# Kernel tuning notes

Measured on AMD Instinct MI355X. Metric: run time of the kernel, lower is better.

The kernel has to match this reference:

```python
import jax, jax.numpy as jnp
import numpy as np

D_MODEL = 1024
N_HEAD = 16
D_K = D_MODEL // N_HEAD
B, S = 2, 2048


def setup_inputs() -> dict:
    key = jax.random.key(0)
    ks = jax.random.split(key, 12)
    sc = 1.0 / np.sqrt(D_MODEL)
    return {
        "q": jax.random.normal(ks[0], (B, S, D_MODEL), jnp.float32),
        "k": jax.random.normal(ks[1], (B, S, D_MODEL), jnp.float32),
        "v": jax.random.normal(ks[2], (B, S, D_MODEL), jnp.float32),
        "mask": jax.random.randint(ks[3], (B, S, S), 0, 2, jnp.int32),
        # learned params (torch Linear convention: y = x @ W + b with W pre-transposed)
        "wq": jax.random.normal(ks[4], (D_MODEL, D_MODEL), jnp.float32) * sc,
        "bq": jax.random.normal(ks[5], (D_MODEL,), jnp.float32) * sc,
        "wk": jax.random.normal(ks[6], (D_MODEL, D_MODEL), jnp.float32) * sc,  # no bias
        "wv": jax.random.normal(ks[7], (D_MODEL, D_MODEL), jnp.float32) * sc,
        "bv": jax.random.normal(ks[8], (D_MODEL,), jnp.float32) * sc,
        "wf": jax.random.normal(ks[9], (D_MODEL, D_MODEL), jnp.float32) * sc,
        "bf": jax.random.normal(ks[10], (D_MODEL,), jnp.float32) * sc,
    }


def reference(q, k, v, mask, wq, bq, wk, wv, bv, wf, bf):
    bs = q.shape[0]
    temperature = jnp.asarray(D_K ** 0.5, q.dtype)
    # projections -> [b, h, s, d_k]
    qh = (q @ wq + bq).reshape(bs, -1, N_HEAD, D_K).transpose(0, 2, 1, 3)
    kh = (k @ wk).reshape(bs, -1, N_HEAD, D_K).transpose(0, 2, 1, 3)
    vh = (v @ wv + bv).reshape(bs, -1, N_HEAD, D_K).transpose(0, 2, 1, 3)
    # scores [b, h, sq, sk]
    attn = jnp.einsum("bhqd,bhkd->bhqk", qh, kh) / temperature
    m0 = (mask[:, None, :, :] == 0)  # mask==0 -> masked out, broadcast over heads
    attn = jnp.where(m0, -jnp.inf, attn)
    attn = jax.nn.softmax(attn, axis=-1)
    attn = jnp.where(m0, 0.0, attn)
    out = jnp.einsum("bhqk,bhkd->bhqd", attn, vh)
    out = out.transpose(0, 2, 1, 3).reshape(bs, -1, D_MODEL)
    return out @ wf + bf  # dropout is identity in eval mode
```

## Files before the change

### kernel.cpp

```cpp
#include <hip/hip_runtime.h>

#define D_MODEL 1024
#define NHEAD   16
#define DK      64
#define BATCH   2
#define SEQ     2048

typedef __attribute__((ext_vector_type(8))) short bf16x8;
typedef __attribute__((ext_vector_type(4))) short bf16x4;
typedef __attribute__((ext_vector_type(4))) float f32x4;
typedef __attribute__((ext_vector_type(2))) int i32x2;

#define QSCALE 0.18033688011f

__device__ __forceinline__ unsigned short f2b(float x) {
  unsigned u = __builtin_bit_cast(unsigned, x);
  u = (u + 0x7fffu + ((u >> 16) & 1u)) >> 16;
  return (unsigned short)u;
}
__device__ __forceinline__ unsigned short f2b_rhu(float x) {
  return (unsigned short)((__builtin_bit_cast(unsigned, x) + 0x8000u) >> 16);
}
__device__ __forceinline__ int pk2(float a, float b) {
  unsigned ua = __builtin_bit_cast(unsigned, a) + 0x8000u;
  unsigned ub = __builtin_bit_cast(unsigned, b) + 0x8000u;
  return (int)__builtin_amdgcn_perm(ub, ua, 0x07060302u);
}
__device__ __forceinline__ int pk2u(unsigned ua, unsigned ub) {
  return (int)__builtin_amdgcn_perm(ub + 0x8000u, ua + 0x8000u, 0x07060302u);
}

typedef const __attribute__((address_space(1))) void* gas_p;
typedef __attribute__((address_space(3))) void* las_p;
__device__ __forceinline__ void gll16(const void* g, void* l) {
  __builtin_amdgcn_global_load_lds((gas_p)g, (las_p)l, 16, 0, 0);
}

__device__ __forceinline__ f32x4 mfma16(bf16x4 a, bf16x4 b, f32x4 c) {
#if __has_builtin(__builtin_amdgcn_mfma_f32_16x16x16bf16_1k)
  return __builtin_amdgcn_mfma_f32_16x16x16bf16_1k(a, b, c, 0, 0, 0);
#else
  f32x4 d;
  asm("v_mfma_f32_16x16x16_bf16 %0, %1, %2, %3" : "=v"(d) : "v"(a), "v"(b), "v"(c));
  return d;
#endif
}

__global__ __launch_bounds__(256) void prep_kernel(
    const float* __restrict__ q, const float* __restrict__ k, const float* __restrict__ v,
    unsigned short* __restrict__ qb, unsigned short* __restrict__ kb,
    unsigned short* __restrict__ vb,
    const float* __restrict__ wq, const float* __restrict__ wk,
    const float* __restrict__ wv, const float* __restrict__ wf,
    unsigned short* __restrict__ wqt, unsigned short* __restrict__ wkt,
    unsigned short* __restrict__ wvt, unsigned short* __restrict__ wft,
    const int* __restrict__ mask, unsigned long long* __restrict__ mbits) {
  int bid = blockIdx.x, t = threadIdx.x;
  if (bid < 6144) {
    int by = bid >> 11, bx = bid & 2047;
    const float* src = by == 0 ? q : (by == 1 ? k : v);
    unsigned short* dst = by == 0 ? qb : (by == 1 ? kb : vb);
    size_t i = ((size_t)bx * 256 + t) * 8;
    float4 x0 = *(const float4*)&src[i];
    float4 x1 = *(const float4*)&src[i + 4];
    int4 w;
    w.x = pk2(x0.x, x0.y); w.y = pk2(x0.z, x0.w);
    w.z = pk2(x1.x, x1.y); w.w = pk2(x1.z, x1.w);
    *(int4*)&dst[i] = w;
  } else if (bid < 7168) {
    __shared__ float tile[64][65];
    int idx = bid - 6144;
    int bz = idx >> 8, by = (idx >> 4) & 15, bx = idx & 15;
    const float* w; unsigned short* wt;
    switch (bz) {
      case 0: w = wq; wt = wqt; break;
      case 1: w = wk; wt = wkt; break;
      case 2: w = wv; wt = wvt; break;
      default: w = wf; wt = wft; break;
    }
    int r0 = by * 64, c0 = bx * 64;
    for (int i = 0; i < 16; ++i) {
      int idx2 = t + i * 256; int r = idx2 >> 6, c = idx2 & 63;
      tile[r][c] = w[(size_t)(r0 + r) * D_MODEL + c0 + c];
    }
    __syncthreads();
    for (int i = 0; i < 16; ++i) {
      int idx2 = t + i * 256; int r = idx2 >> 6, c = idx2 & 63;
      wt[(size_t)(c0 + r) * D_MODEL + r0 + c] = f2b(tile[c][r]);
    }
  } else {
    int idx = bid - 7168;
    int lane = t & 63, wave = t >> 6;
    size_t base = ((size_t)idx * 4 + wave) * 256;
    unsigned long long b0 = __ballot(mask[base + lane] != 0);
    unsigned long long b1 = __ballot(mask[base + 64 + lane] != 0);
    unsigned long long b2 = __ballot(mask[base + 128 + lane] != 0);
    unsigned long long b3 = __ballot(mask[base + 192 + lane] != 0);
    if (lane == 0) {
      unsigned long long* p = &mbits[(size_t)idx * 16 + wave * 4];
      p[0] = b0; p[1] = b1; p[2] = b2; p[3] = b3;
    }
  }
}

__global__ __launch_bounds__(256) void gemm_qkv_kernel(
    const unsigned short* __restrict__ qb, const unsigned short* __restrict__ kb,
    const unsigned short* __restrict__ vb,
    const unsigned short* __restrict__ wqt, const unsigned short* __restrict__ wkt,
    const unsigned short* __restrict__ wvt,
    const float* __restrict__ bq, const float* __restrict__ bv,
    unsigned short* __restrict__ qh, unsigned short* __restrict__ kh,
    unsigned short* __restrict__ vt) {
  __shared__ unsigned short SB[16640];
  int bid = blockIdx.x;
  int xcd = bid & 7, slot = bid >> 3;
  int mi = slot & 3, zn = slot >> 2;
  int z = zn >> 3;
  int n0 = (zn & 7) * 128;
  int m0 = (mi * 8 + xcd) * 128;
  const unsigned short* A; const unsigned short* Bt;
  switch (z) {
    case 0:  A = qb; Bt = wqt; break;
    case 1:  A = kb; Bt = wkt; break;
    default: A = vb; Bt = wvt; break;
  }
  int t = threadIdx.x, lane = t & 63, wave = t >> 6;
  int l16 = lane & 15, quad = lane >> 4;
  int wm = (wave & 1) * 64, wn = (wave >> 1) * 64;
  f32x4 zero = {0.f, 0.f, 0.f, 0.f};
  f32x4 acc[4][4];
  for (int mt = 0; mt < 4; ++mt) for (int nt = 0; nt < 4; ++nt) acc[mt][nt] = zero;

  int drow = lane >> 2, dcol = (lane & 3) * 8;
  const unsigned short* asrc = A  + (size_t)(m0 + wave * 32 + drow) * D_MODEL + dcol;
  const unsigned short* bsrc = Bt + (size_t)(n0 + wave * 32 + drow) * D_MODEL + dcol;
  int dst = wave * 1024 + lane * 8;

#pragma unroll
  for (int g = 0; g < 2; ++g) {
    gll16(asrc + (size_t)(g * 16) * D_MODEL, &SB[dst + g * 512]);
    gll16(bsrc + (size_t)(g * 16) * D_MODEL, &SB[4096 + dst + g * 512]);
  }
  for (int it = 0; it < 32; ++it) {
    __syncthreads();
    if (it + 1 < 32) {
      int nb = ((it + 1) & 1) * 8192, kn = (it + 1) * 32;
#pragma unroll
      for (int g = 0; g < 2; ++g) {
        gll16(asrc + (size_t)(g * 16) * D_MODEL + kn, &SB[nb + dst + g * 512]);
        gll16(bsrc + (size_t)(g * 16) * D_MODEL + kn, &SB[nb + 4096 + dst + g * 512]);
      }
    }
    int cb = (it & 1) * 8192;
    bf16x8 a[4], b[4];
    for (int mt = 0; mt < 4; ++mt)
      a[mt] = *(const bf16x8*)&SB[cb + (wm + mt * 16 + l16) * 32 + quad * 8];
    for (int nt = 0; nt < 4; ++nt)
      b[nt] = *(const bf16x8*)&SB[cb + 4096 + (wn + nt * 16 + l16) * 32 + quad * 8];
    for (int mt = 0; mt < 4; ++mt)
      for (int nt = 0; nt < 4; ++nt)
        acc[mt][nt] = __builtin_amdgcn_mfma_f32_16x16x32_bf16(a[mt], b[nt], acc[mt][nt], 0, 0, 0);
  }

  if (z == 2) {
    __syncthreads();
#pragma unroll
    for (int nt = 0; nt < 4; ++nt) {
      int col = wn + nt * 16 + l16;
      float bb = bv[n0 + col];
      for (int mt = 0; mt < 4; ++mt)
        for (int r = 0; r < 4; ++r)
          SB[col * 130 + wm + mt * 16 + quad * 4 + r] = f2b_rhu(acc[mt][nt][r] + bb);
    }
    __syncthreads();
    int c = t >> 1, hf = t & 1;
    int colg = n0 + c, hh = colg >> 6, dd = colg & 63;
    int b_ = m0 >> 11, sbase = m0 & (SEQ - 1);
    unsigned short* dstp = vt + (((size_t)(b_ * NHEAD + hh)) * DK + dd) * SEQ + sbase + hf * 64;
#pragma unroll
    for (int j = 0; j < 8; ++j)
      *(int4*)(dstp + j * 8) = *(const int4*)&SB[c * 130 + hf * 64 + j * 8];
  } else {
    __syncthreads();
#pragma unroll
    for (int nt = 0; nt < 4; ++nt) {
      int lcol = wn + nt * 16 + l16;
      float bb = (z == 0) ? bq[n0 + lcol] : 0.f;
      for (int mt = 0; mt < 4; ++mt)
        for (int r = 0; r < 4; ++r) {
          float val = acc[mt][nt][r] + bb;
          if (z == 0) val *= QSCALE;
          SB[(wm + mt * 16 + quad * 4 + r) * 130 + lcol] = f2b_rhu(val);
        }
    }
    __syncthreads();
    unsigned short* outp = (z == 0) ? qh : kh;
    int b_ = m0 >> 11, sbase = m0 & (SEQ - 1);
    int h0 = n0 >> 6, c = t & 7;
#pragma unroll
    for (int pass = 0; pass < 8; ++pass) {
      int rp = pass * 32 + (t >> 3);
      int srow = rp >> 1, part = rp & 1;
      unsigned short* dstp = outp +
          (((size_t)(b_ * NHEAD + h0 + part)) * SEQ + sbase + srow) * DK + c * 8;
      *(int4*)dstp = *(const int4*)&SB[srow * 130 + part * 64 + c * 8];
    }
  }
}

__global__ __launch_bounds__(256) void gemm_out_kernel(
    const unsigned short* __restrict__ A, const unsigned short* __restrict__ Bt,
    const float* __restrict__ bias, float* __restrict__ out) {
  __shared__ unsigned short As[8192], Bs[8192];
  int bid = blockIdx.x;
  int xcd = bid & 7, slot = bid >> 3;
  int mi = slot & 7, n0 = (slot >> 3) * 64;
  int m0 = (mi * 8 + xcd) * 64;
  int t = threadIdx.x, lane = t & 63, wave = t >> 6;
  int l16 = lane & 15, quad = lane >> 4;
  int wm = (wave & 1) * 32, wn = (wave >> 1) * 32;
  f32x4 zero = {0.f, 0.f, 0.f, 0.f};
  f32x4 acc[2][2];
  for (int mt = 0; mt < 2; ++mt) for (int nt = 0; nt < 2; ++nt) acc[mt][nt] = zero;

  int drow = lane >> 2, dcol = (lane & 3) * 8;
  const unsigned short* asrc = A  + (size_t)(m0 + wave * 16 + drow) * D_MODEL + dcol;
  const unsigned short* bsrc = Bt + (size_t)(n0 + wave * 16 + drow) * D_MODEL + dcol;
  int dst = wave * 512 + lane * 8;

#pragma unroll
  for (int hf = 0; hf < 2; ++hf) {
    gll16(asrc + hf * 32, &As[dst + hf * 2048]);
    gll16(bsrc + hf * 32, &Bs[dst + hf * 2048]);
  }
  for (int it = 0; it < 16; ++it) {
    __syncthreads();
    if (it + 1 < 16) {
      int nb = ((it + 1) & 1) * 4096, kn = (it + 1) * 64;
#pragma unroll
      for (int hf = 0; hf < 2; ++hf) {
        gll16(asrc + kn + hf * 32, &As[nb + dst + hf * 2048]);
        gll16(bsrc + kn + hf * 32, &Bs[nb + dst + hf * 2048]);
      }
    }
    int cb = (it & 1) * 4096;
#pragma unroll
    for (int half = 0; half < 2; ++half) {
      bf16x8 a[2], b[2];
      for (int mt = 0; mt < 2; ++mt)
        a[mt] = *(const bf16x8*)&As[cb + half * 2048 + (wm + mt * 16 + l16) * 32 + quad * 8];
      for (int nt = 0; nt < 2; ++nt)
        b[nt] = *(const bf16x8*)&Bs[cb + half * 2048 + (wn + nt * 16 + l16) * 32 + quad * 8];
      for (int mt = 0; mt < 2; ++mt)
        for (int nt = 0; nt < 2; ++nt)
          acc[mt][nt] = __builtin_amdgcn_mfma_f32_16x16x32_bf16(a[mt], b[nt], acc[mt][nt], 0, 0, 0);
    }
  }
  for (int nt = 0; nt < 2; ++nt) {
    int col = n0 + wn + nt * 16 + l16;
    float bb = bias[col];
    for (int mt = 0; mt < 2; ++mt)
      for (int r = 0; r < 4; ++r) {
        int row = m0 + wm + mt * 16 + quad * 4 + r;
        out[(size_t)row * D_MODEL + col] = acc[mt][nt][r] + bb;
      }
  }
}

__global__ __launch_bounds__(256, 2) void attn_kernel(
    const unsigned short* __restrict__ qh, const unsigned short* __restrict__ kh,
    const unsigned short* __restrict__ vt, const unsigned long long* __restrict__ mbits,
    unsigned short* __restrict__ attb) {
  __shared__ unsigned short Ks[16384];
  __shared__ unsigned short Vs[16384];
  int bid = blockIdx.x;
  int xcd = bid & 7, slot = bid >> 3;
  int bh_ = 4 * xcd + (slot >> 4);
  int qt = slot & 15;
  int b = bh_ >> 4, h = bh_ & 15;
  int t = threadIdx.x, lane = t & 63, wave = t >> 6;
  int l16 = lane & 15, quad = lane >> 4;
  size_t bh = (size_t)b * NHEAD + h;

  const unsigned short* Kg = kh + bh * SEQ * DK;
  const unsigned short* Vg = vt + bh * DK * SEQ;
  const unsigned long long* mrow = mbits + (size_t)b * SEQ * (SEQ / 64);
  int qrowb = qt * 128 + wave * 32;

  bf16x8 qf[2][2];
#pragma unroll
  for (int qm = 0; qm < 2; ++qm) {
    const unsigned short* Qg = qh + (bh * SEQ + (size_t)(qrowb + qm * 16 + l16)) * DK;
    qf[qm][0] = *(const bf16x8*)&Qg[quad * 8];
    qf[qm][1] = *(const bf16x8*)&Qg[32 + quad * 8];
  }

  int ksrow = t >> 3;
  int kschk = ((t & 7) ^ (ksrow & 7)) * 8;
  const unsigned short* ksrc = Kg + (size_t)ksrow * DK + kschk;
  int vsrow = t >> 4;
  int vschk = ((t & 15) ^ (vsrow & 15)) * 8;
  const unsigned short* vsrc = Vg + (size_t)vsrow * SEQ + vschk;
  int sdst = t * 8;

  int x7 = l16 & 7;
  int ka0 = l16 * 64 + ((quad ^ x7) * 8);
  int ka1 = l16 * 64 + (((4 + quad) ^ x7) * 8);
  int va[2][4];
#pragma unroll
  for (int sub = 0; sub < 2; ++sub)
#pragma unroll
    for (int nt = 0; nt < 4; ++nt)
      va[sub][nt] = l16 * 128 + (((sub * 8 + nt * 2 + (quad >> 1)) ^ l16) * 8)
                    + (quad & 1) * 4;

  size_t mi0 = (size_t)(qrowb + l16) * (SEQ / 64);
  size_t mi1 = (size_t)(qrowb + 16 + l16) * (SEQ / 64);

  bf16x4 ones4;
#pragma unroll
  for (int i = 0; i < 4; ++i) ones4[i] = (short)0x3F80;

  f32x4 zero = {0.f, 0.f, 0.f, 0.f};
  f32x4 accO[2][4], accRS[2];
#pragma unroll
  for (int qm = 0; qm < 2; ++qm) {
    accRS[qm] = zero;
    for (int dt = 0; dt < 4; ++dt) accO[qm][dt] = zero;
  }

#pragma unroll
  for (int g = 0; g < 4; ++g) {
    gll16(ksrc + (size_t)(g * 32) * DK, &Ks[g * 2048 + sdst]);
    gll16(vsrc + (size_t)(g * 16) * SEQ, &Vs[g * 2048 + sdst]);
  }

  for (int tk = 0; tk < SEQ / 128; ++tk) {
    __syncthreads();
    if (tk + 1 < SEQ / 128) {
      int nb = ((tk + 1) & 1) * 8192;
      const unsigned short* kn = ksrc + (size_t)(tk + 1) * 128 * DK;
      const unsigned short* vn = vsrc + (tk + 1) * 128;
#pragma unroll
      for (int g = 0; g < 4; ++g) {
        gll16(kn + (size_t)(g * 32) * DK, &Ks[nb + g * 2048 + sdst]);
        gll16(vn + (size_t)(g * 16) * SEQ, &Vs[nb + g * 2048 + sdst]);
      }
    }
    unsigned long long mA0 = mrow[mi0 + 2 * tk];
    unsigned long long mA1 = mrow[mi0 + 2 * tk + 1];
    unsigned long long mB0 = mrow[mi1 + 2 * tk];
    unsigned long long mB1 = mrow[mi1 + 2 * tk + 1];

    int cb = (tk & 1) * 8192;
#pragma unroll
    for (int sub = 0; sub < 2; ++sub) {
      int kb_ = cb + sub * 4096;
      f32x4 accS[2][4];
#pragma unroll
      for (int qm = 0; qm < 2; ++qm)
        for (int nt = 0; nt < 4; ++nt) accS[qm][nt] = zero;
#pragma unroll
      for (int step = 0; step < 2; ++step) {
        int ka = step ? ka1 : ka0;
#pragma unroll
        for (int nt = 0; nt < 4; ++nt) {
          bf16x8 kf = *(const bf16x8*)&Ks[kb_ + ka + nt * 1024];
          accS[0][nt] = __builtin_amdgcn_mfma_f32_16x16x32_bf16(kf, qf[0][step], accS[0][nt], 0, 0, 0);
          accS[1][nt] = __builtin_amdgcn_mfma_f32_16x16x32_bf16(kf, qf[1][step], accS[1][nt], 0, 0, 0);
        }
      }

      unsigned long long ms0 = sub ? mA1 : mA0;
      unsigned long long ms1 = sub ? mB1 : mB0;
      bf16x4 ap[2][4];
#pragma unroll
      for (int qm = 0; qm < 2; ++qm) {
        unsigned long long mq = (qm ? ms1 : ms0) >> (quad * 4);
        unsigned mlo = (unsigned)mq, mhi = (unsigned)(mq >> 32);
#pragma unroll
        for (int nt = 0; nt < 4; ++nt) {
          unsigned w = (nt < 2) ? mlo : mhi;
          unsigned pu[4];
#pragma unroll
          for (int r = 0; r < 4; ++r) {
            float pv = __builtin_amdgcn_exp2f(accS[qm][nt][r]);
            int msk = ((int)(w << (31 - ((nt & 1) * 16 + r)))) >> 31;
            pu[r] = __builtin_bit_cast(unsigned, pv) & (unsigned)msk;
          }
          i32x2 wv;
          wv[0] = pk2u(pu[0], pu[1]);
          wv[1] = pk2u(pu[2], pu[3]);
          ap[qm][nt] = __builtin_bit_cast(bf16x4, wv);
        }
#pragma unroll
        for (int nt = 0; nt < 4; ++nt)
          accRS[qm] = mfma16(ap[qm][nt], ones4, accRS[qm]);
      }

#pragma unroll
      for (int nt = 0; nt < 4; ++nt) {
        int vb_ = cb + va[sub][nt];
#pragma unroll
        for (int dt = 0; dt < 4; ++dt) {
          bf16x4 vf = *(const bf16x4*)&Vs[vb_ + dt * 2048];
          accO[0][dt] = mfma16(ap[0][nt], vf, accO[0][dt]);
          accO[1][dt] = mfma16(ap[1][nt], vf, accO[1][dt]);
        }
      }
    }
  }

#pragma unroll
  for (int qm = 0; qm < 2; ++qm)
    for (int r = 0; r < 4; ++r) {
      float sden = accRS[qm][r];
      float inv = sden > 0.f ? 1.f / sden : 0.f;
      int row = qrowb + qm * 16 + quad * 4 + r;
      size_t ob = ((size_t)b * SEQ + row) * D_MODEL + (size_t)h * DK;
      for (int dt = 0; dt < 4; ++dt)
        attb[ob + dt * 16 + l16] = f2b_rhu(accO[qm][dt][r] * inv);
    }
}

extern "C" void kernel_launch(void* const* d_in, const int* in_sizes, int n_in,
                              void* d_out, int out_size, void* d_ws, size_t ws_size,
                              hipStream_t stream) {
  (void)in_sizes; (void)n_in; (void)out_size; (void)ws_size;
  const float* q    = (const float*)d_in[0];
  const float* k    = (const float*)d_in[1];
  const float* v    = (const float*)d_in[2];
  const int*   mask = (const int*)d_in[3];
  const float* wq   = (const float*)d_in[4];
  const float* bq   = (const float*)d_in[5];
  const float* wk   = (const float*)d_in[6];
  const float* wv   = (const float*)d_in[7];
  const float* bv   = (const float*)d_in[8];
  const float* wf   = (const float*)d_in[9];
  const float* bf   = (const float*)d_in[10];

  char* ws = (char*)d_ws;
  unsigned short* wft  = (unsigned short*)(ws + 0);
  unsigned short* wqt  = (unsigned short*)(ws + 2097152);
  unsigned short* wkt  = (unsigned short*)(ws + 4194304);
  unsigned short* wvt  = (unsigned short*)(ws + 6291456);
  unsigned short* attb = (unsigned short*)(ws + 2097152);
  unsigned short* qhp  = (unsigned short*)(ws + 10485760);
  unsigned short* khp  = (unsigned short*)(ws + 18874368);
  unsigned short* vtp  = (unsigned short*)(ws + 27262976);
  unsigned long long* mbits = (unsigned long long*)(ws + 35651584);
  unsigned short* vb   = (unsigned short*)(ws + 36700160);
  unsigned short* qb   = (unsigned short*)d_out;
  unsigned short* kb   = (unsigned short*)d_out + 4194304;

  hipLaunchKernelGGL(prep_kernel, dim3(15360), dim3(256), 0, stream,
                     q, k, v, qb, kb, vb,
                     wq, wk, wv, wf, wqt, wkt, wvt, wft, mask, mbits);
  hipLaunchKernelGGL(gemm_qkv_kernel, dim3(768), dim3(256), 0, stream,
                     qb, kb, vb, wqt, wkt, wvt, bq, bv, qhp, khp, vtp);
  hipLaunchKernelGGL(attn_kernel, dim3(512), dim3(256), 0, stream,
                     qhp, khp, vtp, mbits, attb);
  hipLaunchKernelGGL(gemm_out_kernel, dim3(1024), dim3(256), 0, stream,
                     attb, wft, bf, (float*)d_out);
}
```

Before: 261.7 us.

## Split attention block into 8 waves of 16 query rows with MFMA priority hints

The attention kernel now runs 512 threads per block, and each wave owns 16 query rows instead of 32. Register pressure per wave drops, and more waves can hide the latency of the exp/mask and LDS work. K/V tile loads are spread across twice as many threads with fewer load instructions each. s_setprio calls raise wave priority around the MFMA sections so that waves interleave their matrix and vector work. The trade-off is that each K/V fragment read from LDS now feeds only one MFMA instead of two, which doubles LDS read traffic per unit of math.

```diff
diff --git a/kernel.cpp b/kernel.cpp
--- a/kernel.cpp
+++ b/kernel.cpp
@@ -267,7 +267,7 @@
   }
 }
 
-__global__ __launch_bounds__(256, 2) void attn_kernel(
+__global__ __launch_bounds__(512, 4) void attn_kernel(
     const unsigned short* __restrict__ qh, const unsigned short* __restrict__ kh,
     const unsigned short* __restrict__ vt, const unsigned long long* __restrict__ mbits,
     unsigned short* __restrict__ attb) {
@@ -285,14 +285,13 @@
   const unsigned short* Kg = kh + bh * SEQ * DK;
   const unsigned short* Vg = vt + bh * DK * SEQ;
   const unsigned long long* mrow = mbits + (size_t)b * SEQ * (SEQ / 64);
-  int qrowb = qt * 128 + wave * 32;
-
-  bf16x8 qf[2][2];
-#pragma unroll
-  for (int qm = 0; qm < 2; ++qm) {
-    const unsigned short* Qg = qh + (bh * SEQ + (size_t)(qrowb + qm * 16 + l16)) * DK;
-    qf[qm][0] = *(const bf16x8*)&Qg[quad * 8];
-    qf[qm][1] = *(const bf16x8*)&Qg[32 + quad * 8];
+  int qrowb = qt * 128 + wave * 16;
+
+  bf16x8 qf[2];
+  {
+    const unsigned short* Qg = qh + (bh * SEQ + (size_t)(qrowb + l16)) * DK;
+    qf[0] = *(const bf16x8*)&Qg[quad * 8];
+    qf[1] = *(const bf16x8*)&Qg[32 + quad * 8];
   }
 
   int ksrow = t >> 3;
@@ -315,24 +314,20 @@
                     + (quad & 1) * 4;
 
   size_t mi0 = (size_t)(qrowb + l16) * (SEQ / 64);
-  size_t mi1 = (size_t)(qrowb + 16 + l16) * (SEQ / 64);
 
   bf16x4 ones4;
 #pragma unroll
   for (int i = 0; i < 4; ++i) ones4[i] = (short)0x3F80;
 
   f32x4 zero = {0.f, 0.f, 0.f, 0.f};
-  f32x4 accO[2][4], accRS[2];
-#pragma unroll
-  for (int qm = 0; qm < 2; ++qm) {
-    accRS[qm] = zero;
-    for (int dt = 0; dt < 4; ++dt) accO[qm][dt] = zero;
-  }
-
-#pragma unroll
-  for (int g = 0; g < 4; ++g) {
-    gll16(ksrc + (size_t)(g * 32) * DK, &Ks[g * 2048 + sdst]);
-    gll16(vsrc + (size_t)(g * 16) * SEQ, &Vs[g * 2048 + sdst]);
+  f32x4 accO[4], accRS = zero;
+#pragma unroll
+  for (int dt = 0; dt < 4; ++dt) accO[dt] = zero;
+
+#pragma unroll
+  for (int g = 0; g < 2; ++g) {
+    gll16(ksrc + (size_t)(g * 64) * DK, &Ks[g * 4096 + sdst]);
+    gll16(vsrc + (size_t)(g * 32) * SEQ, &Vs[g * 4096 + sdst]);
   }
 
   for (int tk = 0; tk < SEQ / 128; ++tk) {
@@ -342,85 +337,78 @@
       const unsigned short* kn = ksrc + (size_t)(tk + 1) * 128 * DK;
       const unsigned short* vn = vsrc + (tk + 1) * 128;
 #pragma unroll
-      for (int g = 0; g < 4; ++g) {
-        gll16(kn + (size_t)(g * 32) * DK, &Ks[nb + g * 2048 + sdst]);
-        gll16(vn + (size_t)(g * 16) * SEQ, &Vs[nb + g * 2048 + sdst]);
+      for (int g = 0; g < 2; ++g) {
+        gll16(kn + (size_t)(g * 64) * DK, &Ks[nb + g * 4096 + sdst]);
+        gll16(vn + (size_t)(g * 32) * SEQ, &Vs[nb + g * 4096 + sdst]);
       }
     }
     unsigned long long mA0 = mrow[mi0 + 2 * tk];
     unsigned long long mA1 = mrow[mi0 + 2 * tk + 1];
-    unsigned long long mB0 = mrow[mi1 + 2 * tk];
-    unsigned long long mB1 = mrow[mi1 + 2 * tk + 1];
 
     int cb = (tk & 1) * 8192;
 #pragma unroll
     for (int sub = 0; sub < 2; ++sub) {
       int kb_ = cb + sub * 4096;
-      f32x4 accS[2][4];
-#pragma unroll
-      for (int qm = 0; qm < 2; ++qm)
-        for (int nt = 0; nt < 4; ++nt) accS[qm][nt] = zero;
+      f32x4 accS[4];
+#pragma unroll
+      for (int nt = 0; nt < 4; ++nt) accS[nt] = zero;
+      __builtin_amdgcn_s_setprio(1);
 #pragma unroll
       for (int step = 0; step < 2; ++step) {
         int ka = step ? ka1 : ka0;
 #pragma unroll
         for (int nt = 0; nt < 4; ++nt) {
           bf16x8 kf = *(const bf16x8*)&Ks[kb_ + ka + nt * 1024];
-          accS[0][nt] = __builtin_amdgcn_mfma_f32_16x16x32_bf16(kf, qf[0][step], accS[0][nt], 0, 0, 0);
-          accS[1][nt] = __builtin_amdgcn_mfma_f32_16x16x32_bf16(kf, qf[1][step], accS[1][nt], 0, 0, 0);
+          accS[nt] = __builtin_amdgcn_mfma_f32_16x16x32_bf16(kf, qf[step], accS[nt], 0, 0, 0);
         }
       }
-
-      unsigned long long ms0 = sub ? mA1 : mA0;
-      unsigned long long ms1 = sub ? mB1 : mB0;
-      bf16x4 ap[2][4];
-#pragma unroll
-      for (int qm = 0; qm < 2; ++qm) {
-        unsigned long long mq = (qm ? ms1 : ms0) >> (quad * 4);
-        unsigned mlo = (unsigned)mq, mhi = (unsigned)(mq >> 32);
-#pragma unroll
-        for (int nt = 0; nt < 4; ++nt) {
-          unsigned w = (nt < 2) ? mlo : mhi;
-          unsigned pu[4];
-#pragma unroll
-          for (int r = 0; r < 4; ++r) {
-            float pv = __builtin_amdgcn_exp2f(accS[qm][nt][r]);
-            int msk = ((int)(w << (31 - ((nt & 1) * 16 + r)))) >> 31;
-            pu[r] = __builtin_bit_cast(unsigned, pv) & (unsigned)msk;
-          }
-          i32x2 wv;
-          wv[0] = pk2u(pu[0], pu[1]);
-          wv[1] = pk2u(pu[2], pu[3]);
-          ap[qm][nt] = __builtin_bit_cast(bf16x4, wv);
+      __builtin_amdgcn_s_setprio(0);
+
+      unsigned long long mq = (sub ? mA1 : mA0) >> (quad * 4);
+      unsigned mlo = (unsigned)mq, mhi = (unsigned)(mq >> 32);
+      bf16x4 ap[4];
+#pragma unroll
+      for (int nt = 0; nt < 4; ++nt) {
+        unsigned w = (nt < 2) ? mlo : mhi;
+        unsigned pu[4];
+#pragma unroll
+        for (int r = 0; r < 4; ++r) {
+          float pv = __builtin_amdgcn_exp2f(accS[nt][r]);
+          int msk = ((int)(w << (31 - ((nt & 1) * 16 + r)))) >> 31;
+          pu[r] = __builtin_bit_cast(unsigned, pv) & (unsigned)msk;
         }
-#pragma unroll
-        for (int nt = 0; nt < 4; ++nt)
-          accRS[qm] = mfma16(ap[qm][nt], ones4, accRS[qm]);
-      }
-
+        i32x2 wv;
+        wv[0] = pk2u(pu[0], pu[1]);
+        wv[1] = pk2u(pu[2], pu[3]);
+        ap[nt] = __builtin_bit_cast(bf16x4, wv);
+      }
+
+      __builtin_amdgcn_s_setprio(1);
+#pragma unroll
+      for (int nt = 0; nt < 4; ++nt)
+        accRS = mfma16(ap[nt], ones4, accRS);
 #pragma unroll
       for (int nt = 0; nt < 4; ++nt) {
         int vb_ = cb + va[sub][nt];
 #pragma unroll
         for (int dt = 0; dt < 4; ++dt) {
           bf16x4 vf = *(const bf16x4*)&Vs[vb_ + dt * 2048];
-          accO[0][dt] = mfma16(ap[0][nt], vf, accO[0][dt]);
-          accO[1][dt] = mfma16(ap[1][nt], vf, accO[1][dt]);
+          accO[dt] = mfma16(ap[nt], vf, accO[dt]);
         }
       }
-    }
-  }
-
-#pragma unroll
-  for (int qm = 0; qm < 2; ++qm)
-    for (int r = 0; r < 4; ++r) {
-      float sden = accRS[qm][r];
-      float inv = sden > 0.f ? 1.f / sden : 0.f;
-      int row = qrowb + qm * 16 + quad * 4 + r;
-      size_t ob = ((size_t)b * SEQ + row) * D_MODEL + (size_t)h * DK;
-      for (int dt = 0; dt < 4; ++dt)
-        attb[ob + dt * 16 + l16] = f2b_rhu(accO[qm][dt][r] * inv);
-    }
+      __builtin_amdgcn_s_setprio(0);
+    }
+  }
+
+#pragma unroll
+  for (int r = 0; r < 4; ++r) {
+    float sden = accRS[r];
+    float inv = sden > 0.f ? 1.f / sden : 0.f;
+    int row = qrowb + quad * 4 + r;
+    size_t ob = ((size_t)b * SEQ + row) * D_MODEL + (size_t)h * DK;
+    for (int dt = 0; dt < 4; ++dt)
+      attb[ob + dt * 16 + l16] = f2b_rhu(accO[dt][r] * inv);
+  }
 }
 
 extern "C" void kernel_launch(void* const* d_in, const int* in_sizes, int n_in,
@@ -458,7 +446,7 @@
                      wq, wk, wv, wf, wqt, wkt, wvt, wft, mask, mbits);
   hipLaunchKernelGGL(gemm_qkv_kernel, dim3(768), dim3(256), 0, stream,
                      qb, kb, vb, wqt, wkt, wvt, bq, bv, qhp, khp, vtp);
-  hipLaunchKernelGGL(attn_kernel, dim3(512), dim3(256), 0, stream,
+  hipLaunchKernelGGL(attn_kernel, dim3(512), dim3(512), 0, stream,
                      qhp, khp, vtp, mbits, attb);
   hipLaunchKernelGGL(gemm_out_kernel, dim3(1024), dim3(256), 0, stream,
                      attb, wft, bf, (float*)d_out);
```

Measured after the change: 250.1 us. -4.4%, faster.
